# Performance work log

Hardware: AMD Instinct MI355X
Metric: run time of the kernel (lower is better)

Reference implementation:

```python
import jax, jax.numpy as jnp
import numpy as np
import math

PSIZE = [(8, 8), (16, 16)]


def _conv2d(x, w, b):
    # 3x3 stride-1 'SAME' conv, NCHW / OIHW
    y = jax.lax.conv_general_dilated(
        x, w, window_strides=(1, 1), padding='SAME',
        dimension_numbers=('NCHW', 'OIHW', 'NCHW'))
    return y + b[None, :, None, None]


def _patch_attention(x, xs, b, t, c, h, w, ph, pw):
    oh, ow = h // ph, w // pw
    d = c * ph * pw
    # query: [b, oh*ow, c*ph*pw]
    q = x.reshape(b, c, oh, ph, ow, pw).transpose(0, 2, 4, 1, 3, 5).reshape(b, oh * ow, d)
    # key/value: [b, t*oh*ow, c*ph*pw]
    k = xs.reshape(b, t, c, oh, ph, ow, pw).transpose(0, 1, 3, 5, 2, 4, 6).reshape(b, t * oh * ow, d)
    scores = jnp.einsum('bqd,bkd->bqk', q, k) / jnp.asarray(math.sqrt(d), x.dtype)
    # NOTE: the original torch code calls scores.masked_fill(mm, -1e9) without
    # assigning the result, so the mask has NO effect; we faithfully omit it.
    atten = jax.nn.softmax(scores, axis=-1)
    val = jnp.einsum('bqk,bkd->bqd', atten, k)
    y = val.reshape(b, oh, ow, c, ph, pw).transpose(0, 3, 1, 4, 2, 5).reshape(b, c, h, w)
    return y


def setup_inputs() -> dict:
    key = jax.random.key(0)
    ks = jax.random.split(key, 6)
    b, t, c, h, w = 2, 5, 256, 128, 128
    n_p = len(PSIZE)
    x = jax.random.normal(ks[0], (b, c, h, w), dtype=jnp.float32)
    xs = jax.random.normal(ks[1], (b * t, c, h, w), dtype=jnp.float32)
    ms = jax.random.uniform(ks[2], (b * t, 1, h, w), dtype=jnp.float32)
    fan_lin = c * n_p * 9
    w_lin = jax.random.normal(ks[3], (c, c * n_p, 3, 3), dtype=jnp.float32) * (1.0 / math.sqrt(fan_lin))
    b_lin = jnp.zeros((c,), dtype=jnp.float32)
    fan_g = 512 * 9
    w_gate = jax.random.normal(ks[4], (c, 2 * c, 3, 3), dtype=jnp.float32) * (1.0 / math.sqrt(fan_g))
    b_gate = jnp.zeros((c,), dtype=jnp.float32)
    w_feat = jax.random.normal(ks[5], (c, 2 * c, 3, 3), dtype=jnp.float32) * (1.0 / math.sqrt(fan_g))
    b_feat = jnp.zeros((c,), dtype=jnp.float32)
    return {'x': x, 'xs': xs, 'ms': ms, 'w_lin': w_lin, 'b_lin': b_lin,
            'w_gate': w_gate, 'b_gate': b_gate, 'w_feat': w_feat, 'b_feat': b_feat}


def reference(x, xs, ms, w_lin, b_lin, w_gate, b_gate, w_feat, b_feat):
    b, c, h, w = x.shape
    t = xs.shape[0] // b
    outs = [_patch_attention(x, xs, b, t, c, h, w, ph, pw) for (ph, pw) in PSIZE]
    out = jnp.concatenate(outs, axis=1)                    # [b, c*len(psize), h, w]
    out = jax.nn.leaky_relu(_conv2d(out, w_lin, b_lin), 0.2)  # [b, c, h, w]
    fused = jnp.concatenate([x, out], axis=1)              # [b, 2c, h, w]
    gating = _conv2d(fused, w_gate, b_gate)
    feature = jax.nn.leaky_relu(_conv2d(fused, w_feat, b_feat), 0.2)
    x_out = jax.nn.sigmoid(gating) * feature               # [b, c, h, w]
    return x_out
```

## Files before the change

### kernel.cpp

```cpp
#include <hip/hip_runtime.h>

typedef unsigned short u16;
typedef unsigned int u32;
typedef __attribute__((ext_vector_type(8))) short bf16x8;
typedef __attribute__((ext_vector_type(4))) float f32x4;

#define MFMA16(d, a, bb) d = __builtin_amdgcn_mfma_f32_16x16x32_bf16(a, bb, d, 0, 0, 0)

__device__ __forceinline__ float bf2f(u16 u){
  union { u32 i; float f; } v; v.i = ((u32)u) << 16; return v.f;
}
__device__ __forceinline__ u16 f2bf(float f){
  union { float f; u32 i; } v; v.f = f;
  u32 r = v.i + 0x7fffu + ((v.i >> 16) & 1u);
  return (u16)(r >> 16);
}
__device__ __forceinline__ void unpack8(uint4 v, float* dst){
  dst[0]=bf2f((u16)(v.x & 0xffff)); dst[1]=bf2f((u16)(v.x >> 16));
  dst[2]=bf2f((u16)(v.y & 0xffff)); dst[3]=bf2f((u16)(v.y >> 16));
  dst[4]=bf2f((u16)(v.z & 0xffff)); dst[5]=bf2f((u16)(v.z >> 16));
  dst[6]=bf2f((u16)(v.w & 0xffff)); dst[7]=bf2f((u16)(v.w >> 16));
}

__device__ __forceinline__ void gl16(const u16* g, u16* l){
  __builtin_amdgcn_global_load_lds(
      (const __attribute__((address_space(1))) u32*)g,
      (__attribute__((address_space(3))) u32*)l, 16, 0, 0);
}

__global__ __launch_bounds__(64) void k_zero(u32* zp){
  zp[threadIdx.x] = 0u;
}

__global__ __launch_bounds__(256) void k_transpose(const float* __restrict__ in,
                                                   u16* __restrict__ out,
                                                   int rows, int cols,
                                                   int ostride, size_t o_imgstride){
  __shared__ float s[32][33];
  const float* ip = in + (size_t)blockIdx.z * (size_t)rows * (size_t)cols;
  u16* op = out + (size_t)blockIdx.z * o_imgstride;
  int r0 = blockIdx.x * 32, c0 = blockIdx.y * 32;
  int tx = threadIdx.x, ty = threadIdx.y;
#pragma unroll
  for(int i = 0; i < 4; ++i){
    int r = ty * 4 + i;
    s[r][tx] = ip[(size_t)(r0 + r) * cols + (c0 + tx)];
  }
  __syncthreads();
#pragma unroll
  for(int i = 0; i < 4; ++i){
    int c = ty * 4 + i;
    op[(size_t)(c0 + c) * ostride + (r0 + tx)] = f2bf(s[tx][c]);
  }
}

__global__ __launch_bounds__(256) void k_wt(const float* __restrict__ in,
                                            u16* __restrict__ out,
                                            int co_mul, int co_off, int co_tot){
  int ci = blockIdx.x * 256 + threadIdx.x;
  int co = blockIdx.y;
  int e  = blockIdx.z;
  out[((size_t)e * co_tot + co * co_mul + co_off) * 512 + ci] =
      f2bf(in[((size_t)co * 512 + ci) * 9 + e]);
}

__global__ __launch_bounds__(256) void k_scores8(const u16* __restrict__ FUSED,
                                                 const u16* __restrict__ XST,
                                                 float* __restrict__ S8p){
  __shared__ u16 As[4096], Bs[4096];
  const int bz = blockIdx.z, b = bz >> 3, g = bz & 7;
  const int q0 = blockIdx.x * 128, k0 = blockIdx.y * 128;
  const int tid = threadIdx.x, w = tid >> 6, l = tid & 63;
  const int wr = w >> 1, wc = w & 1;
  const int l15 = l & 15, kg = (l >> 4) * 8;
  f32x4 acc[4][4];
#pragma unroll
  for(int m = 0; m < 4; ++m)
#pragma unroll
    for(int n = 0; n < 4; ++n) acc[m][n] = (f32x4){0.f, 0.f, 0.f, 0.f};

  for(int e8 = 0; e8 < 8; ++e8){
    const int e = g * 8 + e8, dy = e >> 3, dx = e & 7;
    for(int ci0 = 0; ci0 < 256; ci0 += 32){
#pragma unroll
      for(int r = 0; r < 2; ++r){
        const int idx = (w * 2 + r) * 64 + l;
        const int q = q0 + (idx >> 2);
        const size_t pa = ((size_t)b * 16384 +
                           (size_t)(((q >> 4) << 3) + dy) * 128 + ((q & 15) << 3) + dx) * 512
                          + ci0 + (idx & 3) * 8;
        gl16(FUSED + pa, As + (size_t)(w * 2 + r) * 512);
        const int k = k0 + (idx >> 2), t = k >> 8, rm = k & 255;
        const size_t pb = (((size_t)b * 5 + t) * 16384 +
                           (size_t)(((rm >> 4) << 3) + dy) * 128 + ((rm & 15) << 3) + dx) * 256
                          + ci0 + (idx & 3) * 8;
        gl16(XST + pb, Bs + (size_t)(w * 2 + r) * 512);
      }
      __syncthreads();
      bf16x8 af[4], bq[4];
#pragma unroll
      for(int m = 0; m < 4; ++m) af[m] = *(const bf16x8*)(As + (wr * 64 + m * 16 + l15) * 32 + kg);
#pragma unroll
      for(int n = 0; n < 4; ++n) bq[n] = *(const bf16x8*)(Bs + (wc * 64 + n * 16 + l15) * 32 + kg);
#pragma unroll
      for(int m = 0; m < 4; ++m)
#pragma unroll
        for(int n = 0; n < 4; ++n)
          acc[m][n] = __builtin_amdgcn_mfma_f32_16x16x32_bf16(af[m], bq[n], acc[m][n], 0, 0, 0);
      __syncthreads();
    }
  }
  float* dst = S8p + ((size_t)g * 2 + b) * 256 * 1280;
#pragma unroll
  for(int m = 0; m < 4; ++m){
    const int q = q0 + wr * 64 + m * 16 + (l >> 4) * 4;
#pragma unroll
    for(int n = 0; n < 4; ++n){
      const int k = k0 + wc * 64 + n * 16 + l15;
#pragma unroll
      for(int r = 0; r < 4; ++r) dst[(size_t)(q + r) * 1280 + k] = acc[m][n][r];
    }
  }
}

__global__ __launch_bounds__(256) void k_softmax8(const float* __restrict__ S8p,
                                                  u16* __restrict__ A8){
  __shared__ float red[8];
  int b = blockIdx.x >> 8, q = blockIdx.x & 255;
  size_t roff = ((size_t)b * 256 + q) * 1280;
  int tid = threadIdx.x;
  float v[5]; float m = -1e30f;
#pragma unroll
  for(int i = 0; i < 5; ++i){
    size_t o = roff + tid + 256 * i;
    float s = 0.f;
#pragma unroll
    for(int g = 0; g < 8; ++g) s += S8p[(size_t)g * 655360 + o];
    v[i] = s * 0.0078125f; m = fmaxf(m, v[i]);
  }
#pragma unroll
  for(int o = 32; o > 0; o >>= 1) m = fmaxf(m, __shfl_xor(m, o));
  int wid = tid >> 6;
  if((tid & 63) == 0) red[wid] = m;
  __syncthreads();
  m = fmaxf(fmaxf(red[0], red[1]), fmaxf(red[2], red[3]));
  float s = 0.f;
#pragma unroll
  for(int i = 0; i < 5; ++i){ v[i] = __expf(v[i] - m); s += v[i]; }
#pragma unroll
  for(int o = 32; o > 0; o >>= 1) s += __shfl_xor(s, o);
  if((tid & 63) == 0) red[4 + wid] = s;
  __syncthreads();
  s = red[4] + red[5] + red[6] + red[7];
  float inv = 1.0f / s;
#pragma unroll
  for(int i = 0; i < 5; ++i) A8[roff + tid + 256 * i] = f2bf(v[i] * inv);
}

__global__ __launch_bounds__(320) void k_s16(const float* __restrict__ S8p,
                                             float* __restrict__ A16){
  __shared__ float red[10];
  int b = blockIdx.x >> 6, q16 = blockIdx.x & 63;
  int tid = threadIdx.x;
  int t = tid >> 6, rm = tid & 63;
  int KY = rm >> 3, KX = rm & 7;
  int QY = q16 >> 3, QX = q16 & 7;
  float s = 0.f;
#pragma unroll
  for(int i = 0; i < 2; ++i)
#pragma unroll
    for(int j = 0; j < 2; ++j){
      int q8 = (2 * QY + i) * 16 + (2 * QX + j);
      int k8 = t * 256 + (2 * KY + i) * 16 + (2 * KX + j);
      size_t o = ((size_t)b * 256 + q8) * 1280 + k8;
#pragma unroll
      for(int g = 0; g < 8; ++g) s += S8p[(size_t)g * 655360 + o];
    }
  s *= 0.00390625f;
  float m = s;
#pragma unroll
  for(int o = 32; o > 0; o >>= 1) m = fmaxf(m, __shfl_xor(m, o));
  int wid = tid >> 6;
  if((tid & 63) == 0) red[wid] = m;
  __syncthreads();
  m = fmaxf(fmaxf(fmaxf(red[0], red[1]), fmaxf(red[2], red[3])), red[4]);
  float e = __expf(s - m);
  float sm = e;
#pragma unroll
  for(int o = 32; o > 0; o >>= 1) sm += __shfl_xor(sm, o);
  if((tid & 63) == 0) red[5 + wid] = sm;
  __syncthreads();
  sm = red[5] + red[6] + red[7] + red[8] + red[9];
  A16[((size_t)b * 64 + q16) * 320 + tid] = e / sm;
}

__global__ __launch_bounds__(256) void k_val8(const u16* __restrict__ A8,
                                              const u16* __restrict__ XST,
                                              u16* __restrict__ OUTCAT){
  __shared__ u16 As[4096];
  __shared__ u16 Bs[128 * 40];
  const int z = blockIdx.z, b = z >> 6, rr = z & 63;
  const int ry = rr >> 3, rx = rr & 7;
  const int q0 = blockIdx.x * 128, c0 = blockIdx.y * 128;
  const int tid = threadIdx.x, w = tid >> 6, l = tid & 63;
  const int wr = w >> 1, wc = w & 1;
  const int l15 = l & 15, kg = (l >> 4) * 8;
  const int k2 = tid >> 4, ch8 = tid & 15;
  f32x4 acc[4][4];
#pragma unroll
  for(int m = 0; m < 4; ++m)
#pragma unroll
    for(int n = 0; n < 4; ++n) acc[m][n] = (f32x4){0.f, 0.f, 0.f, 0.f};

  for(int k0 = 0; k0 < 1280; k0 += 32){
#pragma unroll
    for(int r = 0; r < 2; ++r){
      const int idx = (w * 2 + r) * 64 + l;
      const u16* ga = A8 + ((size_t)b * 256 + q0 + (idx >> 2)) * 1280 + k0 + (idx & 3) * 8;
      gl16(ga, As + (size_t)(w * 2 + r) * 512);
    }
    {
      const int ka = k0 + k2 * 2, kb = ka + 1;
      const int ta = ka >> 8, ra = ka & 255;
      const int tb = kb >> 8, rb = kb & 255;
      const size_t pa = (((size_t)b * 5 + ta) * 16384 +
                         (size_t)(((ra >> 4) << 3) + ry) * 128 + ((ra & 15) << 3) + rx) * 256
                        + c0 + ch8 * 8;
      const size_t pb = (((size_t)b * 5 + tb) * 16384 +
                         (size_t)(((rb >> 4) << 3) + ry) * 128 + ((rb & 15) << 3) + rx) * 256
                        + c0 + ch8 * 8;
      union { uint4 v; u16 s[8]; } u0, u1;
      u0.v = *(const uint4*)(XST + pa);
      u1.v = *(const uint4*)(XST + pb);
      const int kloc = k2 * 2, swz = (ch8 & 3) << 3;
#pragma unroll
      for(int j = 0; j < 8; ++j){
        u32 pack = (u32)u0.s[j] | ((u32)u1.s[j] << 16);
        *(u32*)(Bs + (size_t)(ch8 * 8 + j) * 40 + (kloc ^ swz)) = pack;
      }
    }
    __syncthreads();
    bf16x8 af[4], bq[4];
#pragma unroll
    for(int m = 0; m < 4; ++m) af[m] = *(const bf16x8*)(As + (wr * 64 + m * 16 + l15) * 32 + kg);
#pragma unroll
    for(int n = 0; n < 4; ++n){
      const int ch = wc * 64 + n * 16 + l15;
      bq[n] = *(const bf16x8*)(Bs + (size_t)ch * 40 + (kg ^ (((ch >> 3) & 3) << 3)));
    }
#pragma unroll
    for(int m = 0; m < 4; ++m)
#pragma unroll
      for(int n = 0; n < 4; ++n)
        acc[m][n] = __builtin_amdgcn_mfma_f32_16x16x32_bf16(af[m], bq[n], acc[m][n], 0, 0, 0);
    __syncthreads();
  }
#pragma unroll
  for(int m = 0; m < 4; ++m){
    const int qb = q0 + wr * 64 + m * 16 + (l >> 4) * 4;
#pragma unroll
    for(int n = 0; n < 4; ++n){
      const int ch = c0 + wc * 64 + n * 16 + l15;
#pragma unroll
      for(int r = 0; r < 4; ++r){
        const int q = qb + r;
        const int py = ((q >> 4) << 3) + ry, px = ((q & 15) << 3) + rx;
        OUTCAT[((size_t)b * 16384 + (size_t)py * 128 + px) * 512 + ch] = f2bf(acc[m][n][r]);
      }
    }
  }
}

__global__ __launch_bounds__(256) void k_val16(const float* __restrict__ A16,
                                               const u16* __restrict__ XST,
                                               u16* __restrict__ OUTCAT){
  __shared__ float As[64][68], Bs[64][68];
  int z = blockIdx.z; int b = z >> 8, rr = z & 255;
  int ry = rr >> 4, rx = rr & 15;
  int c0 = blockIdx.y * 64;
  int tid = threadIdx.x;
  int row = tid >> 2, quarter = tid & 3;
  int qg = tid >> 4, cg = tid & 15;
  float acc[4][4] = {{0.f}};
  for(int k0 = 0; k0 < 320; k0 += 64){
    {
      const float* src = A16 + ((size_t)b * 64 + row) * 320 + k0 + quarter * 16;
      float4 v0 = ((const float4*)src)[0];
      float4 v1 = ((const float4*)src)[1];
      float4 v2 = ((const float4*)src)[2];
      float4 v3 = ((const float4*)src)[3];
      float4* d = (float4*)&As[row][quarter * 16];
      d[0] = v0; d[1] = v1; d[2] = v2; d[3] = v3;
    }
    {
      int k = k0 + row;
      int t = k >> 6, rm = k & 63;
      int py = ((rm >> 3) << 4) + ry, px = ((rm & 7) << 4) + rx;
      const uint4* s4 = (const uint4*)(XST + ((((size_t)b * 5 + t) * 128 + py) * 128 + px) * 256 + c0 + quarter * 16);
      uint4 v0 = s4[0], v1 = s4[1];
      unpack8(v0, &Bs[row][quarter * 16]);
      unpack8(v1, &Bs[row][quarter * 16 + 8]);
    }
    __syncthreads();
#pragma unroll 8
    for(int kk = 0; kk < 64; ++kk){
      float a[4], bb[4];
#pragma unroll
      for(int i = 0; i < 4; ++i) a[i] = As[qg + 16 * i][kk];
#pragma unroll
      for(int j = 0; j < 4; ++j) bb[j] = Bs[kk][cg + 16 * j];
#pragma unroll
      for(int i = 0; i < 4; ++i)
#pragma unroll
        for(int j = 0; j < 4; ++j) acc[i][j] += a[i] * bb[j];
    }
    __syncthreads();
  }
#pragma unroll
  for(int i = 0; i < 4; ++i){
    int q = qg + 16 * i;
    int py = ((q >> 3) << 4) + ry, px = ((q & 7) << 4) + rx;
    u16* dst = OUTCAT + (((size_t)b * 128 + py) * 128 + px) * 512 + 256 + c0;
#pragma unroll
    for(int j = 0; j < 4; ++j) dst[cg + 16 * j] = f2bf(acc[i][j]);
  }
}

template<int MODE>
__global__ __launch_bounds__(512, 2) void k_conv8(const u16* __restrict__ A,
                                                  const u16* __restrict__ W,
                                                  const float* __restrict__ bias,
                                                  const float* __restrict__ bias2,
                                                  void* __restrict__ outp,
                                                  const u16* __restrict__ zp,
                                                  int Ntot){
  constexpr int BM = (MODE == 0) ? 128 : 256;
  constexpr int MF = BM / 32;
  constexpr int AJ = BM / 128;
  constexpr int BUFU = (BM + 256) * 64;
  constexpr int NT = 72;
  __shared__ u16 lds[2][BUFU];
  const int b = blockIdx.z;
  const int m0 = blockIdx.x * BM;
  const int n0 = blockIdx.y * 256;
  const int tid = threadIdx.x, w = tid >> 6, l = tid & 63;
  const int wr = w >> 2, wc = w & 3;
  const int l15 = l & 15, lq = l >> 4;

  f32x4 acc[MF][4];
#pragma unroll
  for(int m = 0; m < MF; ++m)
#pragma unroll
    for(int n = 0; n < 4; ++n) acc[m][n] = (f32x4){0.f, 0.f, 0.f, 0.f};

  auto STAGE_A = [&](int kt, int half){
    const int e = kt >> 3, ci0 = (kt & 7) << 6;
    const int dy = e / 3 - 1, dx = e % 3 - 1;
    u16* dstbase = &lds[kt & 1][0];
#pragma unroll
    for(int j = 0; j < AJ; ++j){
      const int chunk = w * AJ + j;
      const int rowc = half * (BM / 2) + chunk * 8;
      const int row = rowc + (l >> 3);
      const int obs = ((l & 7) * 16) ^ ((row & 7) << 4);
      const int p = m0 + row;
      const int spy = (p >> 7) + dy, spx = (p & 127) + dx;
      const bool inb = ((unsigned)spy < 128u) && ((unsigned)spx < 128u);
      const u16* src = inb ? A + ((size_t)b * 16384 + spy * 128 + spx) * 512 + ci0 + (obs >> 1)
                           : zp;
      gl16(src, dstbase + rowc * 64);
    }
  };
  auto STAGE_B = [&](int kt, int half){
    const int e = kt >> 3, ci0 = (kt & 7) << 6;
    u16* dstbase = &lds[kt & 1][BM * 64];
#pragma unroll
    for(int j = 0; j < 2; ++j){
      const int chunk = w * 2 + j;
      const int rowc = half * 128 + chunk * 8;
      const int row = rowc + (l >> 3);
      const int obs = ((l & 7) * 16) ^ ((row & 7) << 4);
      const int co = n0 + row;
      const u16* src = W + ((size_t)e * Ntot + co) * 512 + ci0 + (obs >> 1);
      gl16(src, dstbase + rowc * 64);
    }
  };

  STAGE_B(0, 0); STAGE_B(0, 1); STAGE_A(0, 0); STAGE_A(0, 1);
  STAGE_B(1, 0); STAGE_B(1, 1); STAGE_A(1, 0);
  if constexpr (MODE == 0) asm volatile("s_waitcnt vmcnt(5)" ::: "memory");
  else                     asm volatile("s_waitcnt vmcnt(6)" ::: "memory");
  __builtin_amdgcn_s_barrier();

  for(int t = 0; t < NT; ++t){
    const char* bufA = (const char*)&lds[t & 1][0];
    const char* bufB = bufA + BM * 128;
    bf16x8 af[MF], bq0[4], bq1[4];
#pragma unroll
    for(int m = 0; m < MF; ++m){
      const int row = wr * (BM / 2) + m * 16 + l15;
      af[m] = *(const bf16x8*)(bufA + row * 128 + ((lq * 16) ^ ((row & 7) << 4)));
    }
#pragma unroll
    for(int n = 0; n < 4; ++n){
      const int row = wc * 64 + n * 16 + l15;
      const int sz = (row & 7) << 4;
      bq0[n] = *(const bf16x8*)(bufB + row * 128 + ((lq * 16) ^ sz));
      bq1[n] = *(const bf16x8*)(bufB + row * 128 + ((64 + lq * 16) ^ sz));
    }
    if(t + 1 < NT) STAGE_A(t + 1, 1);
    asm volatile("s_waitcnt lgkmcnt(0)" ::: "memory");
    __builtin_amdgcn_sched_barrier(0);
    __builtin_amdgcn_s_setprio(1);
#pragma unroll
    for(int m = 0; m < MF; ++m){
      MFMA16(acc[m][0], af[m], bq0[0]);
      MFMA16(acc[m][1], af[m], bq0[1]);
    }
    __builtin_amdgcn_s_setprio(0);
    __builtin_amdgcn_s_barrier();
    if(t + 2 < NT) STAGE_B(t + 2, 0);
    __builtin_amdgcn_s_setprio(1);
#pragma unroll
    for(int m = 0; m < MF; ++m){
      MFMA16(acc[m][2], af[m], bq0[2]);
      MFMA16(acc[m][3], af[m], bq0[3]);
    }
    __builtin_amdgcn_s_setprio(0);
    __builtin_amdgcn_s_barrier();
#pragma unroll
    for(int m = 0; m < MF; ++m){
      const int row = wr * (BM / 2) + m * 16 + l15;
      af[m] = *(const bf16x8*)(bufA + row * 128 + ((64 + lq * 16) ^ ((row & 7) << 4)));
    }
    if(t + 2 < NT) STAGE_B(t + 2, 1);
    asm volatile("s_waitcnt lgkmcnt(0)" ::: "memory");
    __builtin_amdgcn_sched_barrier(0);
    __builtin_amdgcn_s_setprio(1);
#pragma unroll
    for(int m = 0; m < MF; ++m){
      MFMA16(acc[m][0], af[m], bq1[0]);
      MFMA16(acc[m][1], af[m], bq1[1]);
    }
    __builtin_amdgcn_s_setprio(0);
    __builtin_amdgcn_s_barrier();
    if(t + 2 < NT) STAGE_A(t + 2, 0);
    __builtin_amdgcn_s_setprio(1);
#pragma unroll
    for(int m = 0; m < MF; ++m){
      MFMA16(acc[m][2], af[m], bq1[2]);
      MFMA16(acc[m][3], af[m], bq1[3]);
    }
    __builtin_amdgcn_s_setprio(0);
    if(t < NT - 2){
      if constexpr (MODE == 0) asm volatile("s_waitcnt vmcnt(5)" ::: "memory");
      else                     asm volatile("s_waitcnt vmcnt(6)" ::: "memory");
    } else if(t == NT - 2){
      asm volatile("s_waitcnt vmcnt(0)" ::: "memory");
    }
    __builtin_amdgcn_s_barrier();
  }

  if(MODE == 0){
    u16* ob = (u16*)outp;
#pragma unroll
    for(int m = 0; m < MF; ++m){
      const int p0 = m0 + wr * (BM / 2) + m * 16 + lq * 4;
#pragma unroll
      for(int n = 0; n < 4; ++n){
        const int co = n0 + wc * 64 + n * 16 + l15;
        const float bi = bias[co];
#pragma unroll
        for(int r = 0; r < 4; ++r){
          float v = acc[m][n][r] + bi;
          v = v > 0.f ? v : 0.2f * v;
          ob[((size_t)b * 16384 + p0 + r) * 512 + 256 + co] = f2bf(v);
        }
      }
    }
  } else {
    float* ob = (float*)outp;
#pragma unroll
    for(int m = 0; m < MF; ++m){
      const int p0 = m0 + wr * (BM / 2) + m * 16 + lq * 4;
#pragma unroll
      for(int n = 0; n < 4; ++n){
        const int col = n0 + wc * 64 + n * 16 + l15;
        const int s = col & 1, co = col >> 1;
        const float big = bias[co], bif = bias2[co];
        float res[4];
#pragma unroll
        for(int r = 0; r < 4; ++r){
          const float val = acc[m][n][r];
          const float oth = __shfl_xor(val, 1);
          float gg = s ? oth : val;
          float ff = s ? val : oth;
          gg += big; ff += bif;
          ff = ff > 0.f ? ff : 0.2f * ff;
          res[r] = ff / (1.0f + __expf(-gg));
        }
        if(s == 0){
          float4 v4 = make_float4(res[0], res[1], res[2], res[3]);
          *(float4*)&ob[((size_t)b * 256 + co) * 16384 + p0] = v4;
        }
      }
    }
  }
}

extern "C" void kernel_launch(void* const* d_in, const int* in_sizes, int n_in,
                              void* d_out, int out_size, void* d_ws, size_t ws_size,
                              hipStream_t stream){
  const float* x      = (const float*)d_in[0];
  const float* xs     = (const float*)d_in[1];
  const float* w_lin  = (const float*)d_in[3];
  const float* b_lin  = (const float*)d_in[4];
  const float* w_gate = (const float*)d_in[5];
  const float* b_gate = (const float*)d_in[6];
  const float* w_feat = (const float*)d_in[7];
  const float* b_feat = (const float*)d_in[8];
  float* out = (float*)d_out;

  char* ws = (char*)d_ws;
  size_t off = 0;
  auto alloc = [&](size_t bytes) -> void* {
    void* p = ws + off;
    off += (bytes + 255) & ~(size_t)255;
    return p;
  };
  u16* FUSED  = (u16*)alloc(2ull * 16384 * 512 * 2);
  u16* XST    = (u16*)alloc(10ull * 16384 * 256 * 2);
  u16* WTl    = (u16*)alloc(9ull * 256 * 512 * 2);
  u16* WGF    = (u16*)alloc(9ull * 512 * 512 * 2);
  float* S8p  = (float*)alloc(8ull * 655360 * 4);
  u16* A8     = (u16*)alloc(655360ull * 2);
  float* A16  = (float*)alloc(2ull * 64 * 320 * 4);
  u16* OUTCAT = (u16*)alloc(2ull * 16384 * 512 * 2);
  u16* ZP     = (u16*)alloc(256);

  k_zero<<<1, 64, 0, stream>>>((u32*)ZP);

  dim3 tb(32, 8);
  k_transpose<<<dim3(8, 512, 2),  tb, 0, stream>>>(x,  FUSED, 256, 16384, 512, 8388608ull);
  k_transpose<<<dim3(8, 512, 10), tb, 0, stream>>>(xs, XST,   256, 16384, 256, 4194304ull);

  k_wt<<<dim3(2, 256, 9), 256, 0, stream>>>(w_lin,  WTl, 1, 0, 256);
  k_wt<<<dim3(2, 256, 9), 256, 0, stream>>>(w_gate, WGF, 2, 0, 512);
  k_wt<<<dim3(2, 256, 9), 256, 0, stream>>>(w_feat, WGF, 2, 1, 512);

  k_scores8<<<dim3(2, 10, 16), 256, 0, stream>>>(FUSED, XST, S8p);
  k_softmax8<<<512, 256, 0, stream>>>(S8p, A8);
  k_s16<<<128, 320, 0, stream>>>(S8p, A16);

  k_val8 <<<dim3(2, 2, 128), 256, 0, stream>>>(A8, XST, OUTCAT);
  k_val16<<<dim3(1, 4, 512), 256, 0, stream>>>(A16, XST, OUTCAT);

  k_conv8<0><<<dim3(128, 1, 2), 512, 0, stream>>>(OUTCAT, WTl, b_lin, nullptr,
                                                  (void*)FUSED, ZP, 256);
  k_conv8<1><<<dim3(64, 2, 2), 512, 0, stream>>>(FUSED, WGF, b_gate, b_feat,
                                                 (void*)out, ZP, 512);
}
```

Before: 483.1 us.

## Restructure conv GEMM main loop into M/N quadrant phases with reordered staging

Reorders the implicit-GEMM conv main loop so each K-tile runs as four quadrant phases (M-half x N-half), each using the full 64-wide K slice, instead of two K-halves over all columns. Global-to-LDS staging is remapped so each staged chunk lines up with the quadrant consumed next, letting loads of the next tile overlap with MFMA work on the current one. LDS fragment reads are now split across phases, which is meant to cut register pressure and expose more overlap. The cost is extra barriers per iteration and more delicate waitcnt accounting, which raises the risk of a race.

```diff
diff --git a/kernel.cpp b/kernel.cpp
--- a/kernel.cpp
+++ b/kernel.cpp
@@ -336,6 +336,7 @@
                                                   int Ntot){
   constexpr int BM = (MODE == 0) ? 128 : 256;
   constexpr int MF = BM / 32;
+  constexpr int MH = MF / 2;
   constexpr int AJ = BM / 128;
   constexpr int BUFU = (BM + 256) * 64;
   constexpr int NT = 72;
@@ -359,16 +360,16 @@
     u16* dstbase = &lds[kt & 1][0];
 #pragma unroll
     for(int j = 0; j < AJ; ++j){
-      const int chunk = w * AJ + j;
-      const int rowc = half * (BM / 2) + chunk * 8;
-      const int row = rowc + (l >> 3);
+      const int c = w * AJ + j;
+      const int rc = (c & 1) * (BM / 2) + (c >> 1) * 8 + half * (BM / 4);
+      const int row = rc + (l >> 3);
       const int obs = ((l & 7) * 16) ^ ((row & 7) << 4);
       const int p = m0 + row;
       const int spy = (p >> 7) + dy, spx = (p & 127) + dx;
       const bool inb = ((unsigned)spy < 128u) && ((unsigned)spx < 128u);
       const u16* src = inb ? A + ((size_t)b * 16384 + spy * 128 + spx) * 512 + ci0 + (obs >> 1)
                            : zp;
-      gl16(src, dstbase + rowc * 64);
+      gl16(src, dstbase + rc * 64);
     }
   };
   auto STAGE_B = [&](int kt, int half){
@@ -376,18 +377,18 @@
     u16* dstbase = &lds[kt & 1][BM * 64];
 #pragma unroll
     for(int j = 0; j < 2; ++j){
-      const int chunk = w * 2 + j;
-      const int rowc = half * 128 + chunk * 8;
-      const int row = rowc + (l >> 3);
+      const int c = w * 2 + j;
+      const int rc = (c >> 2) * 64 + half * 32 + (c & 3) * 8;
+      const int row = rc + (l >> 3);
       const int obs = ((l & 7) * 16) ^ ((row & 7) << 4);
       const int co = n0 + row;
       const u16* src = W + ((size_t)e * Ntot + co) * 512 + ci0 + (obs >> 1);
-      gl16(src, dstbase + rowc * 64);
+      gl16(src, dstbase + rc * 64);
     }
   };
 
-  STAGE_B(0, 0); STAGE_B(0, 1); STAGE_A(0, 0); STAGE_A(0, 1);
-  STAGE_B(1, 0); STAGE_B(1, 1); STAGE_A(1, 0);
+  STAGE_A(0, 0); STAGE_B(0, 0); STAGE_B(0, 1); STAGE_A(0, 1);
+  STAGE_B(1, 0); STAGE_B(1, 1); STAGE_A(1, 1);
   if constexpr (MODE == 0) asm volatile("s_waitcnt vmcnt(5)" ::: "memory");
   else                     asm volatile("s_waitcnt vmcnt(6)" ::: "memory");
   __builtin_amdgcn_s_barrier();
@@ -395,67 +396,83 @@
   for(int t = 0; t < NT; ++t){
     const char* bufA = (const char*)&lds[t & 1][0];
     const char* bufB = bufA + BM * 128;
-    bf16x8 af[MF], bq0[4], bq1[4];
-#pragma unroll
-    for(int m = 0; m < MF; ++m){
-      const int row = wr * (BM / 2) + m * 16 + l15;
-      af[m] = *(const bf16x8*)(bufA + row * 128 + ((lq * 16) ^ ((row & 7) << 4)));
-    }
-#pragma unroll
-    for(int n = 0; n < 4; ++n){
-      const int row = wc * 64 + n * 16 + l15;
-      const int sz = (row & 7) << 4;
-      bq0[n] = *(const bf16x8*)(bufB + row * 128 + ((lq * 16) ^ sz));
-      bq1[n] = *(const bf16x8*)(bufB + row * 128 + ((64 + lq * 16) ^ sz));
-    }
-    if(t + 1 < NT) STAGE_A(t + 1, 1);
+    auto LDA = [&](int half, int m, int kk) -> bf16x8 {
+      const int row = wr * (BM / 2) + (half * MH + m) * 16 + l15;
+      return *(const bf16x8*)(bufA + row * 128 + (((kk * 4 + lq) * 16) ^ ((row & 7) << 4)));
+    };
+    auto LDB = [&](int half, int n, int kk) -> bf16x8 {
+      const int row = wc * 64 + (half * 2 + n) * 16 + l15;
+      return *(const bf16x8*)(bufB + row * 128 + (((kk * 4 + lq) * 16) ^ ((row & 7) << 4)));
+    };
+    bf16x8 af[MH][2], bq0[2][2], bq1[2][2];
+#pragma unroll
+    for(int m = 0; m < MH; ++m){ af[m][0] = LDA(0, m, 0); af[m][1] = LDA(0, m, 1); }
+#pragma unroll
+    for(int n = 0; n < 2; ++n){ bq0[n][0] = LDB(0, n, 0); bq0[n][1] = LDB(0, n, 1); }
+    if(t + 1 < NT) STAGE_A(t + 1, 0);
+    if constexpr (MODE == 1) asm volatile("s_waitcnt lgkmcnt(8)" ::: "memory");
+    __builtin_amdgcn_sched_barrier(0);
+    __builtin_amdgcn_s_barrier();
     asm volatile("s_waitcnt lgkmcnt(0)" ::: "memory");
     __builtin_amdgcn_sched_barrier(0);
     __builtin_amdgcn_s_setprio(1);
 #pragma unroll
-    for(int m = 0; m < MF; ++m){
-      MFMA16(acc[m][0], af[m], bq0[0]);
-      MFMA16(acc[m][1], af[m], bq0[1]);
-    }
+    for(int m = 0; m < MH; ++m)
+#pragma unroll
+      for(int n = 0; n < 2; ++n){
+        MFMA16(acc[m][n], af[m][0], bq0[n][0]);
+        MFMA16(acc[m][n], af[m][1], bq0[n][1]);
+      }
     __builtin_amdgcn_s_setprio(0);
     __builtin_amdgcn_s_barrier();
+#pragma unroll
+    for(int n = 0; n < 2; ++n){ bq1[n][0] = LDB(1, n, 0); bq1[n][1] = LDB(1, n, 1); }
     if(t + 2 < NT) STAGE_B(t + 2, 0);
-    __builtin_amdgcn_s_setprio(1);
-#pragma unroll
-    for(int m = 0; m < MF; ++m){
-      MFMA16(acc[m][2], af[m], bq0[2]);
-      MFMA16(acc[m][3], af[m], bq0[3]);
-    }
-    __builtin_amdgcn_s_setprio(0);
-    __builtin_amdgcn_s_barrier();
-#pragma unroll
-    for(int m = 0; m < MF; ++m){
-      const int row = wr * (BM / 2) + m * 16 + l15;
-      af[m] = *(const bf16x8*)(bufA + row * 128 + ((64 + lq * 16) ^ ((row & 7) << 4)));
-    }
-    if(t + 2 < NT) STAGE_B(t + 2, 1);
+    __builtin_amdgcn_sched_barrier(0);
+    __builtin_amdgcn_s_barrier();
     asm volatile("s_waitcnt lgkmcnt(0)" ::: "memory");
     __builtin_amdgcn_sched_barrier(0);
     __builtin_amdgcn_s_setprio(1);
 #pragma unroll
-    for(int m = 0; m < MF; ++m){
-      MFMA16(acc[m][0], af[m], bq1[0]);
-      MFMA16(acc[m][1], af[m], bq1[1]);
-    }
+    for(int m = 0; m < MH; ++m)
+#pragma unroll
+      for(int n = 0; n < 2; ++n){
+        MFMA16(acc[m][2 + n], af[m][0], bq1[n][0]);
+        MFMA16(acc[m][2 + n], af[m][1], bq1[n][1]);
+      }
     __builtin_amdgcn_s_setprio(0);
     __builtin_amdgcn_s_barrier();
-    if(t + 2 < NT) STAGE_A(t + 2, 0);
+#pragma unroll
+    for(int m = 0; m < MH; ++m){ af[m][0] = LDA(1, m, 0); af[m][1] = LDA(1, m, 1); }
+    if(t + 2 < NT) STAGE_B(t + 2, 1);
+    __builtin_amdgcn_sched_barrier(0);
+    __builtin_amdgcn_s_barrier();
+    asm volatile("s_waitcnt lgkmcnt(0)" ::: "memory");
+    __builtin_amdgcn_sched_barrier(0);
     __builtin_amdgcn_s_setprio(1);
 #pragma unroll
-    for(int m = 0; m < MF; ++m){
-      MFMA16(acc[m][2], af[m], bq1[2]);
-      MFMA16(acc[m][3], af[m], bq1[3]);
-    }
+    for(int m = 0; m < MH; ++m)
+#pragma unroll
+      for(int n = 0; n < 2; ++n){
+        MFMA16(acc[MH + m][n], af[m][0], bq0[n][0]);
+        MFMA16(acc[MH + m][n], af[m][1], bq0[n][1]);
+      }
     __builtin_amdgcn_s_setprio(0);
-    if(t < NT - 2){
+    __builtin_amdgcn_s_barrier();
+    if(t + 2 < NT) STAGE_A(t + 2, 1);
+    __builtin_amdgcn_s_setprio(1);
+#pragma unroll
+    for(int m = 0; m < MH; ++m)
+#pragma unroll
+      for(int n = 0; n < 2; ++n){
+        MFMA16(acc[MH + m][2 + n], af[m][0], bq1[n][0]);
+        MFMA16(acc[MH + m][2 + n], af[m][1], bq1[n][1]);
+      }
+    __builtin_amdgcn_s_setprio(0);
+    if(t + 2 < NT){
       if constexpr (MODE == 0) asm volatile("s_waitcnt vmcnt(5)" ::: "memory");
       else                     asm volatile("s_waitcnt vmcnt(6)" ::: "memory");
-    } else if(t == NT - 2){
+    } else if(t + 1 < NT){
       asm volatile("s_waitcnt vmcnt(0)" ::: "memory");
     }
     __builtin_amdgcn_s_barrier();
```

Measured after the change: 487.1 us. About the same (+0.8%).
